# Optimization experiments

Hardware: AMD Instinct MI355X
Metric: run time of the kernel (lower is better)

The kernel has to match this reference:

```python
import jax, jax.numpy as jnp
import numpy as np

N = 50000      # nodes
E = 800000     # edges
IN = 64        # in_feats
HID = 4        # hidden_size
OUT = 64       # out_feats
COORS = 3
EPS = 1e-07
NEG_SLOPE = 0.01  # F.leaky_relu default


def setup_inputs() -> dict:
    key = jax.random.key(0)
    ks = jax.random.split(key, 10)
    feat = jax.random.normal(ks[0], (N, IN), dtype=jnp.float32)
    pos = jax.random.normal(ks[1], (N, COORS), dtype=jnp.float32)
    src = jax.random.randint(ks[2], (E,), 0, N, dtype=jnp.int32)
    dst = jax.random.randint(ks[3], (E,), 0, N, dtype=jnp.int32)
    W_self = jax.random.normal(ks[4], (OUT, IN), dtype=jnp.float32) * 0.1
    W_sp = jax.random.normal(ks[5], (HID * IN, COORS), dtype=jnp.float32) * 0.3
    b_sp = jax.random.normal(ks[6], (HID * IN,), dtype=jnp.float32) * 0.05
    W_neigh = jax.random.normal(ks[7], (OUT, HID * IN), dtype=jnp.float32) * 0.05
    b_neigh = jax.random.normal(ks[8], (OUT,), dtype=jnp.float32) * 0.05
    bias = jnp.zeros((OUT,), dtype=jnp.float32)
    return {"feat": feat, "pos": pos, "src": src, "dst": dst,
            "W_self": W_self, "W_sp": W_sp, "b_sp": b_sp,
            "W_neigh": W_neigh, "b_neigh": b_neigh, "bias": bias}


def reference(feat, pos, src, dst, W_self, W_sp, b_sp, W_neigh, b_neigh, bias):
    # per-edge spatial weighting
    rel = pos[dst] - pos[src]                                   # [E, 3]
    scal = jnp.linalg.norm(rel, axis=1, keepdims=True) + EPS    # [E, 1]
    ws = (rel + 1.0) / scal                                     # [E, 3]
    s = jax.nn.leaky_relu(ws @ W_sp.T + b_sp, NEG_SLOPE)        # [E, HID*IN]
    # modulate gathered src features: reshape(E, IN, HID) * h_src[:, :, None]
    msg = (s.reshape(E, IN, HID) * feat[src][:, :, None]).reshape(E, IN * HID)
    # mean aggregation per destination node (zero for isolated nodes)
    neigh_sum = jax.ops.segment_sum(msg, dst, num_segments=N)   # [N, IN*HID]
    cnt = jax.ops.segment_sum(jnp.ones((E,), feat.dtype), dst, num_segments=N)
    neigh_h = neigh_sum / jnp.maximum(cnt, 1.0)[:, None]
    # output projections
    h_neigh = neigh_h @ W_neigh.T + b_neigh                     # [N, OUT]
    rst = feat @ W_self.T + h_neigh + bias                      # [N, OUT]
    return rst
```

## Files before the change

kernel.cpp:

```cpp
#include <hip/hip_runtime.h>
#include <math.h>

#define N_NODES 50000
#define N_EDGES 800000
#define EPS 1e-7f
#define NEG_SLOPE 0.01f

#define SUBCAP 16
#define GSLOTS 64
#define RSTRIDE 72
#define CSTRIDE 16
#define FEAT_BLOCKS (N_NODES * 64 / 4 / 256)
#define EDGE_BLOCKS4 782
#define ACC_STRIDE 264

typedef __attribute__((ext_vector_type(8))) short short8;
typedef __attribute__((ext_vector_type(4))) float f32x4;

__device__ __forceinline__ unsigned bf16_rne(float x) {
    unsigned u = __float_as_uint(x);
    u += 0x7fffu + ((u >> 16) & 1u);
    return u >> 16;
}
__device__ __forceinline__ unsigned pack_bf16(float a, float b) {
    return bf16_rne(a) | (bf16_rne(b) << 16);
}


__global__ __launch_bounds__(256) void pack_hist_kernel(
    const float* __restrict__ feat, uint2* __restrict__ featb2,
    const float* __restrict__ W_neigh, const float* __restrict__ W_self,
    const float* __restrict__ b_neigh, const float* __restrict__ bias,
    unsigned* __restrict__ wnp, unsigned* __restrict__ wsp, float* __restrict__ bb,
    const int* __restrict__ src, const int* __restrict__ dst,
    int* __restrict__ cnt, unsigned short* __restrict__ gsrcs)
{
    const int bid = blockIdx.x;
    if (bid < FEAT_BLOCKS) {
        const int idx = bid * 256 + threadIdx.x;
        float4 v = reinterpret_cast<const float4*>(feat)[idx];
        featb2[idx] = make_uint2(pack_bf16(v.x, v.y), pack_bf16(v.z, v.w));
        return;
    }
    if (bid == FEAT_BLOCKS) {
        const int t = threadIdx.x;
        const float2* Wn2 = (const float2*)W_neigh;
        const float2* Ws2 = (const float2*)W_self;
        for (int i = t; i < 64 * 128; i += 256) {
            float2 v = Wn2[i];
            wnp[i] = pack_bf16(v.x, v.y);
        }
        for (int i = t; i < 64 * 32; i += 256) {
            float2 v = Ws2[i];
            wsp[i] = pack_bf16(v.x, v.y);
        }
        if (t < 64) bb[t] = b_neigh[t] + bias[t];
        return;
    }
    const int base = (bid - FEAT_BLOCKS - 1) * 1024 + threadIdx.x * 4;
    if (base >= N_EDGES) return;
    const int4 s4 = *reinterpret_cast<const int4*>(src + base);
    const int4 d4 = *reinterpret_cast<const int4*>(dst + base);
#define EDGE_PUT(S, D, SUB)                                                      \
    {                                                                            \
        const int p = atomicAdd(&cnt[(D) * CSTRIDE + (SUB)], 1);                 \
        if (p < SUBCAP)                                                          \
            __builtin_nontemporal_store(                                         \
                (unsigned short)(S),                                             \
                &gsrcs[(size_t)(D) * GSLOTS + (SUB) * SUBCAP + p]);              \
    }
    EDGE_PUT(s4.x, d4.x, 0)
    EDGE_PUT(s4.y, d4.y, 1)
    EDGE_PUT(s4.z, d4.z, 2)
    EDGE_PUT(s4.w, d4.w, 3)
#undef EDGE_PUT
}


__device__ __forceinline__ float featload(const char* fB, unsigned srcoff, int lane2) {
    return __uint_as_float(
        (unsigned)(*(const unsigned short*)(fB + srcoff + lane2)) << 16);
}

__global__ __launch_bounds__(256) void aggregate_project_kernel(
    const unsigned short* __restrict__ featb, const float* __restrict__ W_sp,
    const float* __restrict__ b_sp, const int* __restrict__ cnt,
    const unsigned short* __restrict__ gsrcs, const float* __restrict__ pos,
    const short* __restrict__ wnb, const short* __restrict__ wsb,
    const float* __restrict__ bb, float* __restrict__ out)
{
    __shared__ unsigned short accS[16 * ACC_STRIDE];
    __shared__ uint4 recG[16 * RSTRIDE];

    const int lane = threadIdx.x & 63;
    const int w = threadIdx.x >> 6;
    const int nb = blockIdx.x << 4;
    const char* fB = (const char*)featb;
    const int lane2 = lane << 1;

    float wsp0[4], wsp1[4], wsp2[4], bsp[4];
#pragma unroll
    for (int h = 0; h < 4; ++h) {
        int j = lane * 4 + h;
        wsp0[h] = W_sp[j * 3 + 0];
        wsp1[h] = W_sp[j * 3 + 1];
        wsp2[h] = W_sp[j * 3 + 2];
        bsp[h]  = b_sp[j];
    }

    int dtrue[4], deff[4];
#pragma unroll
    for (int q = 0; q < 4; ++q) {
        const int r = (w << 2) + q;
        const int n = nb + r;
        const int4 c4 = *reinterpret_cast<const int4*>(&cnt[n * CSTRIDE]);
        const int c0 = min(c4.x, SUBCAP), c1 = min(c4.y, SUBCAP),
                  c2 = min(c4.z, SUBCAP), c3 = min(c4.w, SUBCAP);
        dtrue[q] = c4.x + c4.y + c4.z + c4.w;
        const int o1 = c0, o2 = c0 + c1, o3 = o2 + c2;
        deff[q] = o3 + c3;
        const uint4 z = make_uint4(0u, 0u, 0u, 0u);
        recG[r * RSTRIDE + lane] = z;
        if (lane < 8) recG[r * RSTRIDE + 64 + lane] = z;
        const int sub = lane >> 4, p = lane & 15;
        const int cs = (sub == 0) ? c0 : (sub == 1) ? c1 : (sub == 2) ? c2 : c3;
        const int ob = (sub == 0) ? 0 : (sub == 1) ? o1 : (sub == 2) ? o2 : o3;
        if (p < cs) {
            const int s = (int)gsrcs[(size_t)n * GSLOTS + lane];
            const float rx = pos[n * 3 + 0] - pos[s * 3 + 0];
            const float ry = pos[n * 3 + 1] - pos[s * 3 + 1];
            const float rz = pos[n * 3 + 2] - pos[s * 3 + 2];
            const float inv = __builtin_amdgcn_rcpf(
                __builtin_amdgcn_sqrtf(rx * rx + ry * ry + rz * rz) + EPS);
            uint4 rec;
            rec.x = __float_as_uint((rx + 1.f) * inv);
            rec.y = __float_as_uint((ry + 1.f) * inv);
            rec.z = __float_as_uint((rz + 1.f) * inv);
            rec.w = (unsigned)s << 7;
            recG[r * RSTRIDE + ob + p] = rec;
        }
    }

#define MLP_ACC(U, F)                                                              \
    {                                                                              \
        const float wx = __uint_as_float((U).x);                                   \
        const float wy = __uint_as_float((U).y);                                   \
        const float wz = __uint_as_float((U).z);                                   \
        float t0 = fmaf(wx, wsp0[0], fmaf(wy, wsp1[0], fmaf(wz, wsp2[0], bsp[0])));\
        float t1 = fmaf(wx, wsp0[1], fmaf(wy, wsp1[1], fmaf(wz, wsp2[1], bsp[1])));\
        float t2 = fmaf(wx, wsp0[2], fmaf(wy, wsp1[2], fmaf(wz, wsp2[2], bsp[2])));\
        float t3 = fmaf(wx, wsp0[3], fmaf(wy, wsp1[3], fmaf(wz, wsp2[3], bsp[3])));\
        a0 = fmaf(fmaxf(t0, t0 * NEG_SLOPE), (F), a0);                             \
        a1 = fmaf(fmaxf(t1, t1 * NEG_SLOPE), (F), a1);                             \
        a2 = fmaf(fmaxf(t2, t2 * NEG_SLOPE), (F), a2);                             \
        a3 = fmaf(fmaxf(t3, t3 * NEG_SLOPE), (F), a3);                             \
    }

#pragma unroll
    for (int q = 0; q < 4; ++q) {
        const int r = (w << 2) + q;
        const int deg = __builtin_amdgcn_readfirstlane(deff[q]);
        const int dt  = __builtin_amdgcn_readfirstlane(dtrue[q]);
        const uint4* gp = &recG[r * RSTRIDE];

        float a0 = 0.f, a1 = 0.f, a2 = 0.f, a3 = 0.f;

        if (deg > 0) {
            const int dm = deg - 1;
            uint4 u0 = gp[0];
            uint4 u1 = gp[1];
            float f0 = featload(fB, u0.w, lane2);
            float f1 = featload(fB, u1.w, lane2);

            for (int e = 0; e < deg; e += 2) {
                uint4 u2 = gp[e + 2];
                uint4 u3 = gp[e + 3];
                float f2 = featload(fB, u2.w, lane2);
                float f3 = featload(fB, u3.w, lane2);

                MLP_ACC(u0, f0)
                {
                    const float fm = (e + 1 <= dm) ? f1 : 0.f;
                    MLP_ACC(u1, fm)
                }

                u0 = u2; u1 = u3;
                f0 = f2; f1 = f3;
            }
        }

        const float mscale = 1.f / fmaxf((float)dt, 1.f);
        uint2 pv = make_uint2(pack_bf16(a0 * mscale, a1 * mscale),
                              pack_bf16(a2 * mscale, a3 * mscale));
        *reinterpret_cast<uint2*>(&accS[r * ACC_STRIDE + lane * 4]) = pv;
    }
#undef MLP_ACC
    __syncthreads();

    const int mrow = lane & 15;
    const int quad = lane >> 4;
    const int o = (w << 4) + mrow;

    f32x4 acc = {0.f, 0.f, 0.f, 0.f};

    const unsigned short* Ar = &accS[mrow * ACC_STRIDE + quad * 8];
    const short* Br = wnb + o * 256 + quad * 8;
#pragma unroll
    for (int ks = 0; ks < 8; ++ks) {
        short8 a = *reinterpret_cast<const short8*>(Ar + ks * 32);
        short8 b = *reinterpret_cast<const short8*>(Br + ks * 32);
        acc = __builtin_amdgcn_mfma_f32_16x16x32_bf16(a, b, acc, 0, 0, 0);
    }

    const short* Fr = (const short*)featb + (size_t)(nb + mrow) * 64 + quad * 8;
    const short* Sr = wsb + o * 64 + quad * 8;
#pragma unroll
    for (int ks = 0; ks < 2; ++ks) {
        short8 a = *reinterpret_cast<const short8*>(Fr + ks * 32);
        short8 b = *reinterpret_cast<const short8*>(Sr + ks * 32);
        acc = __builtin_amdgcn_mfma_f32_16x16x32_bf16(a, b, acc, 0, 0, 0);
    }

    const float badd = bb[o];
#pragma unroll
    for (int r = 0; r < 4; ++r) {
        out[(size_t)(nb + quad * 4 + r) * 64 + o] = acc[r] + badd;
    }
}


extern "C" void kernel_launch(void* const* d_in, const int* in_sizes, int n_in,
                              void* d_out, int out_size, void* d_ws, size_t ws_size,
                              hipStream_t stream) {
    (void)in_sizes; (void)n_in; (void)out_size; (void)ws_size;
    const float* feat    = (const float*)d_in[0];
    const float* pos     = (const float*)d_in[1];
    const int*   src     = (const int*)d_in[2];
    const int*   dst     = (const int*)d_in[3];
    const float* W_self  = (const float*)d_in[4];
    const float* W_sp    = (const float*)d_in[5];
    const float* b_sp    = (const float*)d_in[6];
    const float* W_neigh = (const float*)d_in[7];
    const float* b_neigh = (const float*)d_in[8];
    const float* bias    = (const float*)d_in[9];
    float* out = (float*)d_out;

    unsigned short* gsrcs  = (unsigned short*)d_ws;
    uint2*          featb2 = (uint2*)(gsrcs + (size_t)N_NODES * GSLOTS);
    unsigned int*   wnp    = (unsigned int*)(featb2 + 800000);
    unsigned int*   wsp    = wnp + 8192;
    float*          bb     = (float*)(wsp + 2048);
    int*            cnt    = (int*)(bb + 64);

    hipMemsetAsync(cnt, 0, (size_t)N_NODES * CSTRIDE * sizeof(int), stream);
    pack_hist_kernel<<<FEAT_BLOCKS + 1 + EDGE_BLOCKS4, 256, 0, stream>>>(
        feat, featb2, W_neigh, W_self, b_neigh, bias, wnp, wsp, bb,
        src, dst, cnt, gsrcs);
    aggregate_project_kernel<<<N_NODES / 16, 256, 0, stream>>>(
        (const unsigned short*)featb2, W_sp, b_sp, cnt, gsrcs, pos,
        (const short*)wnp, (const short*)wsp, bb, out);
}
```

Baseline: 212.7 us.

## Pack edge records to bf16 uint2 with zero-pad node and unroll by four

Shrinks the per-edge LDS record from a 16-byte uint4 to an 8-byte uint2, storing the three spatial weights as bf16 and the source index in the high 16 bits. Adds a zeroed padding feature row so empty slots read zero features, which removes the per-edge tail mask, and deepens the prefetch and unroll from two to four edges. This cuts LDS traffic and loop overhead but rounds the spatial weights to bf16, and with deg at most 64 the unroll can read record slots up to index 67.

Result: no change. 213.1 us (+0.2%).

```diff
diff --git a/kernel.cpp b/kernel.cpp
--- a/kernel.cpp
+++ b/kernel.cpp
@@ -10,6 +10,7 @@
 #define GSLOTS 64
 #define RSTRIDE 72
 #define CSTRIDE 16
+#define ZPAD 50000u
 #define FEAT_BLOCKS (N_NODES * 64 / 4 / 256)
 #define EDGE_BLOCKS4 782
 #define ACC_STRIDE 264
@@ -55,6 +56,7 @@
             wsp[i] = pack_bf16(v.x, v.y);
         }
         if (t < 64) bb[t] = b_neigh[t] + bias[t];
+        if (t < 16) featb2[(size_t)ZPAD * 16 + t] = make_uint2(0u, 0u);
         return;
     }
     const int base = (bid - FEAT_BLOCKS - 1) * 1024 + threadIdx.x * 4;
@@ -77,9 +79,10 @@
 }
 
 
-__device__ __forceinline__ float featload(const char* fB, unsigned srcoff, int lane2) {
-    return __uint_as_float(
-        (unsigned)(*(const unsigned short*)(fB + srcoff + lane2)) << 16);
+__device__ __forceinline__ float featload(const unsigned short* featb, unsigned rec_y,
+                                          int lane) {
+    const unsigned idx = ((rec_y >> 10) & 0x3FFFC0u) + (unsigned)lane;
+    return __uint_as_float((unsigned)featb[idx] << 16);
 }
 
 __global__ __launch_bounds__(256) void aggregate_project_kernel(
@@ -90,13 +93,11 @@
     const float* __restrict__ bb, float* __restrict__ out)
 {
     __shared__ unsigned short accS[16 * ACC_STRIDE];
-    __shared__ uint4 recG[16 * RSTRIDE];
+    __shared__ uint2 recG[16 * RSTRIDE];
 
     const int lane = threadIdx.x & 63;
     const int w = threadIdx.x >> 6;
     const int nb = blockIdx.x << 4;
-    const char* fB = (const char*)featb;
-    const int lane2 = lane << 1;
 
     float wsp0[4], wsp1[4], wsp2[4], bsp[4];
 #pragma unroll
@@ -108,6 +109,7 @@
         bsp[h]  = b_sp[j];
     }
 
+    const uint2 zrec = make_uint2(0u, ZPAD << 16);
     int dtrue[4], deff[4];
 #pragma unroll
     for (int q = 0; q < 4; ++q) {
@@ -119,9 +121,8 @@
         dtrue[q] = c4.x + c4.y + c4.z + c4.w;
         const int o1 = c0, o2 = c0 + c1, o3 = o2 + c2;
         deff[q] = o3 + c3;
-        const uint4 z = make_uint4(0u, 0u, 0u, 0u);
-        recG[r * RSTRIDE + lane] = z;
-        if (lane < 8) recG[r * RSTRIDE + 64 + lane] = z;
+        recG[r * RSTRIDE + lane] = zrec;
+        if (lane < 8) recG[r * RSTRIDE + 64 + lane] = zrec;
         const int sub = lane >> 4, p = lane & 15;
         const int cs = (sub == 0) ? c0 : (sub == 1) ? c1 : (sub == 2) ? c2 : c3;
         const int ob = (sub == 0) ? 0 : (sub == 1) ? o1 : (sub == 2) ? o2 : o3;
@@ -132,20 +133,18 @@
             const float rz = pos[n * 3 + 2] - pos[s * 3 + 2];
             const float inv = __builtin_amdgcn_rcpf(
                 __builtin_amdgcn_sqrtf(rx * rx + ry * ry + rz * rz) + EPS);
-            uint4 rec;
-            rec.x = __float_as_uint((rx + 1.f) * inv);
-            rec.y = __float_as_uint((ry + 1.f) * inv);
-            rec.z = __float_as_uint((rz + 1.f) * inv);
-            rec.w = (unsigned)s << 7;
+            const uint2 rec =
+                make_uint2(pack_bf16((rx + 1.f) * inv, (ry + 1.f) * inv),
+                           bf16_rne((rz + 1.f) * inv) | ((unsigned)s << 16));
             recG[r * RSTRIDE + ob + p] = rec;
         }
     }
 
 #define MLP_ACC(U, F)                                                              \
     {                                                                              \
-        const float wx = __uint_as_float((U).x);                                   \
-        const float wy = __uint_as_float((U).y);                                   \
-        const float wz = __uint_as_float((U).z);                                   \
+        const float wx = __uint_as_float((U).x << 16);                             \
+        const float wy = __uint_as_float((U).x & 0xffff0000u);                     \
+        const float wz = __uint_as_float((U).y << 16);                             \
         float t0 = fmaf(wx, wsp0[0], fmaf(wy, wsp1[0], fmaf(wz, wsp2[0], bsp[0])));\
         float t1 = fmaf(wx, wsp0[1], fmaf(wy, wsp1[1], fmaf(wz, wsp2[1], bsp[1])));\
         float t2 = fmaf(wx, wsp0[2], fmaf(wy, wsp1[2], fmaf(wz, wsp2[2], bsp[2])));\
@@ -161,31 +160,32 @@
         const int r = (w << 2) + q;
         const int deg = __builtin_amdgcn_readfirstlane(deff[q]);
         const int dt  = __builtin_amdgcn_readfirstlane(dtrue[q]);
-        const uint4* gp = &recG[r * RSTRIDE];
+        const uint2* gp = &recG[r * RSTRIDE];
 
         float a0 = 0.f, a1 = 0.f, a2 = 0.f, a3 = 0.f;
 
         if (deg > 0) {
-            const int dm = deg - 1;
-            uint4 u0 = gp[0];
-            uint4 u1 = gp[1];
-            float f0 = featload(fB, u0.w, lane2);
-            float f1 = featload(fB, u1.w, lane2);
-
-            for (int e = 0; e < deg; e += 2) {
-                uint4 u2 = gp[e + 2];
-                uint4 u3 = gp[e + 3];
-                float f2 = featload(fB, u2.w, lane2);
-                float f3 = featload(fB, u3.w, lane2);
+            uint2 u0 = gp[0], u1 = gp[1], u2 = gp[2], u3 = gp[3];
+            float f0 = featload(featb, u0.y, lane);
+            float f1 = featload(featb, u1.y, lane);
+            float f2 = featload(featb, u2.y, lane);
+            float f3 = featload(featb, u3.y, lane);
+
+            for (int e = 0; e < deg; e += 4) {
+                uint2 v0 = gp[e + 4], v1 = gp[e + 5];
+                uint2 v2 = gp[e + 6], v3 = gp[e + 7];
+                float g0 = featload(featb, v0.y, lane);
+                float g1 = featload(featb, v1.y, lane);
+                float g2 = featload(featb, v2.y, lane);
+                float g3 = featload(featb, v3.y, lane);
 
                 MLP_ACC(u0, f0)
-                {
-                    const float fm = (e + 1 <= dm) ? f1 : 0.f;
-                    MLP_ACC(u1, fm)
-                }
-
-                u0 = u2; u1 = u3;
-                f0 = f2; f1 = f3;
+                MLP_ACC(u1, f1)
+                MLP_ACC(u2, f2)
+                MLP_ACC(u3, f3)
+
+                u0 = v0; u1 = v1; u2 = v2; u3 = v3;
+                f0 = g0; f1 = g1; f2 = g2; f3 = g3;
             }
         }
 
@@ -247,7 +247,7 @@
 
     unsigned short* gsrcs  = (unsigned short*)d_ws;
     uint2*          featb2 = (uint2*)(gsrcs + (size_t)N_NODES * GSLOTS);
-    unsigned int*   wnp    = (unsigned int*)(featb2 + 800000);
+    unsigned int*   wnp    = (unsigned int*)(featb2 + 800016);
     unsigned int*   wsp    = wnp + 8192;
     float*          bb     = (float*)(wsp + 2048);
     int*            cnt    = (int*)(bb + 64);
```
